# Performance work log

Hardware: AMD Instinct MI355X
Metric: run time of the kernel (lower is better)

## Reference

```python
import jax, jax.numpy as jnp
import numpy as np

N = 20000
E = 320000
IN_FEATS = 512
H = 4
D_HID = 256
D_OUT = 256
NEG_SLOPE = 0.2


def _gat_layer(h, src, dst, Wsrc, Wdst, al, ar, b, apply_act):
    # h: [N, Fin]; Wsrc/Wdst: [Fin, H*D]; al/ar: [H, D]; b: [H*D]
    Hh, Dd = al.shape
    fs = (h @ Wsrc).reshape(-1, Hh, Dd)  # [N, H, D] src projection
    fd = (h @ Wdst).reshape(-1, Hh, Dd)  # [N, H, D] dst projection
    el = (fs * al).sum(-1)               # [N, H]
    er = (fd * ar).sum(-1)               # [N, H]
    e = jax.nn.leaky_relu(el[src] + er[dst], NEG_SLOPE)  # [E, H]
    m = jax.lax.stop_gradient(jax.ops.segment_max(e, dst, num_segments=N))
    m = jnp.where(jnp.isfinite(m), m, 0.0)
    ex = jnp.exp(e - m[dst])
    den = jax.ops.segment_sum(ex, dst, num_segments=N)  # [N, H]
    alpha = ex / den[dst]                               # edge softmax per dst node
    msg = fs[src] * alpha[:, :, None]                   # [E, H, D]
    out = jax.ops.segment_sum(msg, dst, num_segments=N) + b.reshape(Hh, Dd)
    if apply_act:
        out = jax.nn.relu(out)
    return out  # [N, H, D]


def setup_inputs() -> dict:
    key = jax.random.key(0)
    ks = jax.random.split(key, 20)
    x = jax.random.normal(ks[0], (N, IN_FEATS), dtype=jnp.float32)
    src = jax.random.randint(ks[1], (E,), 0, N, dtype=jnp.int32)
    dst = jax.random.randint(ks[2], (E,), 0, N, dtype=jnp.int32)
    fins = [IN_FEATS, H * D_HID, H * D_HID]
    douts = [D_HID, D_HID, D_OUT]
    inp = {"x": x, "src": src, "dst": dst}
    ki = 3
    for l in range(3):
        fin, do = fins[l], douts[l]
        s = 1.0 / np.sqrt(fin)
        inp[f"Wsrc{l}"] = jax.random.normal(ks[ki], (fin, H * do), dtype=jnp.float32) * s; ki += 1
        inp[f"Wdst{l}"] = jax.random.normal(ks[ki], (fin, H * do), dtype=jnp.float32) * s; ki += 1
        inp[f"al{l}"] = jax.random.normal(ks[ki], (H, do), dtype=jnp.float32) * 0.1; ki += 1
        inp[f"ar{l}"] = jax.random.normal(ks[ki], (H, do), dtype=jnp.float32) * 0.1; ki += 1
        inp[f"b{l}"] = jnp.zeros((H * do,), dtype=jnp.float32)
    return inp


def reference(x, src, dst,
              Wsrc0, Wdst0, al0, ar0, b0,
              Wsrc1, Wdst1, al1, ar1, b1,
              Wsrc2, Wdst2, al2, ar2, b2):
    h = _gat_layer(x, src, dst, Wsrc0, Wdst0, al0, ar0, b0, True).reshape(N, -1)
    h = _gat_layer(h, src, dst, Wsrc1, Wdst1, al1, ar1, b1, True).reshape(N, -1)
    h = _gat_layer(h, src, dst, Wsrc2, Wdst2, al2, ar2, b2, False)  # [N, H, D_OUT]
    return h.mean(axis=1)  # [N, D_OUT]
```

## Files before the change

### kernel.cpp

```cpp
#include <hip/hip_runtime.h>
#include <hip/hip_bf16.h>
#include <math.h>

#define NNODES 20000
#define NPAD   20480
#define NBM    160
#define NEDGES 320000
#define HEADS  4
#define DDIM   256
#define MCOLS  1024

typedef __attribute__((ext_vector_type(8))) short short8;
typedef __attribute__((ext_vector_type(4))) float f32x4;

__device__ __forceinline__ unsigned short f2bf(float f) {
  unsigned u = __float_as_uint(f);
  unsigned r = (u + 0x7fffu + ((u >> 16) & 1u)) >> 16;
  return (unsigned short)r;
}
__device__ __forceinline__ float bf2f(unsigned short h) {
  return __uint_as_float(((unsigned)h) << 16);
}

__device__ __forceinline__ void async_ld16(void* lds, const void* g) {
  __builtin_amdgcn_global_load_lds(
      (const __attribute__((address_space(1))) unsigned int*)g,
      (__attribute__((address_space(3))) unsigned int*)lds, 16, 0, 0);
}

__global__ void k_zero(int* deg, int n) {
  int i = blockIdx.x*blockDim.x + threadIdx.x;
  if (i < n) deg[i] = 0;
}
__global__ void k_hist(const int* __restrict__ dst, int* deg, int e) {
  int i = blockIdx.x*blockDim.x + threadIdx.x;
  if (i < e) atomicAdd(&deg[dst[i]], 1);
}
__global__ void k_scan(const int* __restrict__ deg, int* row_ptr, int* cursor) {
  __shared__ int sm[1024];
  int t = threadIdx.x;
  const int CH = 20;
  int base = t*CH;
  int s = 0;
  #pragma unroll
  for (int i = 0; i < CH; ++i) { int idx = base+i; if (idx < NNODES) s += deg[idx]; }
  int val = s;
  sm[t] = s; __syncthreads();
  for (int off = 1; off < 1024; off <<= 1) {
    int add = (t >= off) ? sm[t-off] : 0;
    __syncthreads();
    val += add; sm[t] = val;
    __syncthreads();
  }
  int run = val - s;
  for (int i = 0; i < CH; ++i) {
    int idx = base+i;
    if (idx < NNODES) { row_ptr[idx] = run; cursor[idx] = run; run += deg[idx]; }
  }
  if (t == 0) row_ptr[NNODES] = NEDGES;
}
__global__ void k_fill(const int* __restrict__ src, const int* __restrict__ dst,
                       int* cursor, int* srcs_sorted, int e) {
  int i = blockIdx.x*blockDim.x + threadIdx.x;
  if (i < e) { int pos = atomicAdd(&cursor[dst[i]], 1); srcs_sorted[pos] = src[i]; }
}

__global__ void k_fold(const float* __restrict__ W, const float* __restrict__ v,
                       float* __restrict__ F, int K) {
  int wave = threadIdx.x >> 6, lane = threadIdx.x & 63;
  int p = blockIdx.x*4 + wave;
  if (p >= K*HEADS) return;
  int k = p >> 2, h = p & 3;
  const float4 wv = *(const float4*)&W[(size_t)k*MCOLS + h*DDIM + lane*4];
  const float4 av = *(const float4*)&v[h*DDIM + lane*4];
  float s = wv.x*av.x + wv.y*av.y + wv.z*av.z + wv.w*av.w;
  for (int off = 32; off; off >>= 1) s += __shfl_xor(s, off);
  if (lane == 0) F[k*HEADS + h] = s;
}

__global__ void k_cvt_a(const float* __restrict__ x, unsigned short* __restrict__ hi,
                        unsigned short* __restrict__ lo, int total, int total_pad) {
  int i = blockIdx.x*blockDim.x + threadIdx.x;
  int idx = i*4;
  if (idx >= total_pad) return;
  float4 v = (idx < total) ? *(const float4*)&x[idx] : make_float4(0.f,0.f,0.f,0.f);
  ushort4 h, l;
  h.x = f2bf(v.x); l.x = f2bf(v.x - bf2f(h.x));
  h.y = f2bf(v.y); l.y = f2bf(v.y - bf2f(h.y));
  h.z = f2bf(v.z); l.z = f2bf(v.z - bf2f(h.z));
  h.w = f2bf(v.w); l.w = f2bf(v.w - bf2f(h.w));
  *(ushort4*)&hi[idx] = h;
  *(ushort4*)&lo[idx] = l;
}

__global__ __launch_bounds__(256) void k_cvt_w(const float* __restrict__ W,
                                               unsigned short* __restrict__ Th, int K) {
  __shared__ float sm[32][33];
  int k0 = blockIdx.y*32, n0 = blockIdx.x*32;
  int t = threadIdx.x;
  int r = t >> 3, c4 = (t & 7)*4;
  *(float4*)&sm[r][c4] = *(const float4*)&W[(size_t)(k0 + r)*MCOLS + n0 + c4];
  __syncthreads();
  ushort4 h;
  h.x = f2bf(sm[c4+0][r]);
  h.y = f2bf(sm[c4+1][r]);
  h.z = f2bf(sm[c4+2][r]);
  h.w = f2bf(sm[c4+3][r]);
  *(ushort4*)&Th[(size_t)(n0 + r)*K + k0 + c4] = h;
}

__global__ void k_eler0(const float* __restrict__ x, const float* __restrict__ Wal,
                        const float* __restrict__ Wred,
                        float* __restrict__ el, float* __restrict__ er) {
  int n = blockIdx.x;
  int h = threadIdx.x >> 6, lane = threadIdx.x & 63;
  float sl = 0.f, sr = 0.f;
  for (int k = lane; k < 512; k += 64) {
    float xv = x[(size_t)n*512 + k];
    sl = fmaf(xv, Wal[k*HEADS + h], sl);
    sr = fmaf(xv, Wred[k*HEADS + h], sr);
  }
  for (int off = 32; off; off >>= 1) { sl += __shfl_xor(sl, off); sr += __shfl_xor(sr, off); }
  if (lane == 0) { el[n*HEADS + h] = sl; er[n*HEADS + h] = sr; }
}

__global__ __launch_bounds__(256, 3) void k_gemm_mfma(
    const unsigned short* __restrict__ Ah, const unsigned short* __restrict__ Al,
    const unsigned short* __restrict__ Bh,
    unsigned short* __restrict__ Fh, int K) {
  __shared__ short sAh[128*32], sAl[128*32], sBh[128*32];
  const int t = threadIdx.x;
  const int w = t >> 6, l = t & 63;
  const int b = blockIdx.x;
  const int xcd = b & 7, kk = b >> 3;
  const int bm = xcd*20 + (kk >> 3), bn = kk & 7;
  const int m0 = (w >> 1) * 64, n0 = (w & 1) * 64;

  f32x4 acc[4][4];
  #pragma unroll
  for (int i = 0; i < 4; ++i)
    #pragma unroll
    for (int j = 0; j < 4; ++j) acc[i][j] = (f32x4){0.f, 0.f, 0.f, 0.f};

  const int srow = t >> 2, koct = (t & 3) * 8;
  const size_t r64 = (size_t)64 * K;
  const unsigned short* gAh = Ah + (size_t)(bm*128 + srow)*K + koct;
  const unsigned short* gAl = Al + (size_t)(bm*128 + srow)*K + koct;
  const unsigned short* gBh = Bh + (size_t)(bn*128 + srow)*K + koct;
  char* lAh = (char*)sAh + w*1024;
  char* lAl = (char*)sAl + w*1024;
  char* lBh = (char*)sBh + w*1024;

  const int fr = l & 15, fq = l >> 4;

  for (int k0 = 0; k0 < K; k0 += 32) {
    async_ld16(lAh,        gAh + k0);
    async_ld16(lAh + 4096, gAh + k0 + r64);
    async_ld16(lAl,        gAl + k0);
    async_ld16(lAl + 4096, gAl + k0 + r64);
    async_ld16(lBh,        gBh + k0);
    async_ld16(lBh + 4096, gBh + k0 + r64);
    __syncthreads();

    short8 bhv[4];
    #pragma unroll
    for (int nt = 0; nt < 4; ++nt)
      bhv[nt] = *(const short8*)&sBh[(n0 + nt*16 + fr)*32 + fq*8];
    #pragma unroll
    for (int mt = 0; mt < 4; ++mt) {
      int off = (m0 + mt*16 + fr)*32 + fq*8;
      short8 ah = *(const short8*)&sAh[off];
      short8 al = *(const short8*)&sAl[off];
      #pragma unroll
      for (int nt = 0; nt < 4; ++nt) {
        acc[mt][nt] = __builtin_amdgcn_mfma_f32_16x16x32_bf16(ah, bhv[nt], acc[mt][nt], 0, 0, 0);
        acc[mt][nt] = __builtin_amdgcn_mfma_f32_16x16x32_bf16(al, bhv[nt], acc[mt][nt], 0, 0, 0);
      }
    }
    __syncthreads();
  }

  #pragma unroll
  for (int mt = 0; mt < 4; ++mt)
    #pragma unroll
    for (int nt = 0; nt < 4; ++nt) {
      size_t base = (size_t)(bm*128 + m0 + mt*16 + fq*4)*MCOLS + bn*128 + n0 + nt*16 + fr;
      Fh[base          ] = f2bf(acc[mt][nt][0]);
      Fh[base + MCOLS  ] = f2bf(acc[mt][nt][1]);
      Fh[base + 2*MCOLS] = f2bf(acc[mt][nt][2]);
      Fh[base + 3*MCOLS] = f2bf(acc[mt][nt][3]);
    }
}

__global__ __launch_bounds__(256) void k_agg_f(
    const unsigned short* __restrict__ fsh, const float* __restrict__ el,
    const float* __restrict__ er, const int* __restrict__ row_ptr,
    const int* __restrict__ srcs, const float* __restrict__ bias,
    const float* __restrict__ WalN, const float* __restrict__ WredN,
    unsigned short* __restrict__ Ahi, unsigned short* __restrict__ Alo,
    float* __restrict__ el_next, float* __restrict__ er_next) {
  __shared__ float red_sm[HEADS][8];
  int n = blockIdx.x;
  int h = threadIdx.x >> 6, lane = threadIdx.x & 63;
  int k0 = h*DDIM + lane*4;
  if (n >= NNODES) {
    ushort4 z = {0,0,0,0};
    *(ushort4*)&Ahi[(size_t)n*MCOLS + k0] = z;
    *(ushort4*)&Alo[(size_t)n*MCOLS + k0] = z;
    return;
  }
  int beg = row_ptr[n], end = row_ptr[n+1];
  float er_nh = er[n*HEADS + h];
  float den = 0.f;
  float4 acc = make_float4(0.f, 0.f, 0.f, 0.f);
  const unsigned short* fbase = fsh + h*DDIM + lane*4;
  int i = beg;
  for (; i + 3 < end; i += 4) {
    int s0 = srcs[i], s1 = srcs[i+1], s2 = srcs[i+2], s3 = srcs[i+3];
    float e0 = el[s0*HEADS + h] + er_nh;
    float e1 = el[s1*HEADS + h] + er_nh;
    float e2 = el[s2*HEADS + h] + er_nh;
    float e3 = el[s3*HEADS + h] + er_nh;
    const ushort4 u0 = *(const ushort4*)&fbase[(size_t)s0*MCOLS];
    const ushort4 u1 = *(const ushort4*)&fbase[(size_t)s1*MCOLS];
    const ushort4 u2 = *(const ushort4*)&fbase[(size_t)s2*MCOLS];
    const ushort4 u3 = *(const ushort4*)&fbase[(size_t)s3*MCOLS];
    e0 = e0 >= 0.f ? e0 : 0.2f*e0;  float w0 = expf(e0);
    e1 = e1 >= 0.f ? e1 : 0.2f*e1;  float w1 = expf(e1);
    e2 = e2 >= 0.f ? e2 : 0.2f*e2;  float w2 = expf(e2);
    e3 = e3 >= 0.f ? e3 : 0.2f*e3;  float w3 = expf(e3);
    den += (w0 + w1) + (w2 + w3);
    acc.x = fmaf(w0, bf2f(u0.x), fmaf(w1, bf2f(u1.x), fmaf(w2, bf2f(u2.x), fmaf(w3, bf2f(u3.x), acc.x))));
    acc.y = fmaf(w0, bf2f(u0.y), fmaf(w1, bf2f(u1.y), fmaf(w2, bf2f(u2.y), fmaf(w3, bf2f(u3.y), acc.y))));
    acc.z = fmaf(w0, bf2f(u0.z), fmaf(w1, bf2f(u1.z), fmaf(w2, bf2f(u2.z), fmaf(w3, bf2f(u3.z), acc.z))));
    acc.w = fmaf(w0, bf2f(u0.w), fmaf(w1, bf2f(u1.w), fmaf(w2, bf2f(u2.w), fmaf(w3, bf2f(u3.w), acc.w))));
  }
  for (; i < end; ++i) {
    int s = srcs[i];
    float e = el[s*HEADS + h] + er_nh;
    e = e >= 0.f ? e : 0.2f*e;
    float wgt = expf(e);
    den += wgt;
    const ushort4 u = *(const ushort4*)&fbase[(size_t)s*MCOLS];
    acc.x = fmaf(wgt, bf2f(u.x), acc.x);
    acc.y = fmaf(wgt, bf2f(u.y), acc.y);
    acc.z = fmaf(wgt, bf2f(u.z), acc.z);
    acc.w = fmaf(wgt, bf2f(u.w), acc.w);
  }
  float inv = den > 0.f ? 1.f/den : 0.f;
  const float4 bv = *(const float4*)&bias[k0];
  float4 o;
  o.x = fmaxf(acc.x*inv + bv.x, 0.f);
  o.y = fmaxf(acc.y*inv + bv.y, 0.f);
  o.z = fmaxf(acc.z*inv + bv.z, 0.f);
  o.w = fmaxf(acc.w*inv + bv.w, 0.f);
  ushort4 hv, lv;
  hv.x = f2bf(o.x); lv.x = f2bf(o.x - bf2f(hv.x));
  hv.y = f2bf(o.y); lv.y = f2bf(o.y - bf2f(hv.y));
  hv.z = f2bf(o.z); lv.z = f2bf(o.z - bf2f(hv.z));
  hv.w = f2bf(o.w); lv.w = f2bf(o.w - bf2f(hv.w));
  *(ushort4*)&Ahi[(size_t)n*MCOLS + k0] = hv;
  *(ushort4*)&Alo[(size_t)n*MCOLS + k0] = lv;
  const float4 a0 = *(const float4*)&WalN[(k0+0)*HEADS];
  const float4 a1 = *(const float4*)&WalN[(k0+1)*HEADS];
  const float4 a2 = *(const float4*)&WalN[(k0+2)*HEADS];
  const float4 a3 = *(const float4*)&WalN[(k0+3)*HEADS];
  const float4 q0 = *(const float4*)&WredN[(k0+0)*HEADS];
  const float4 q1 = *(const float4*)&WredN[(k0+1)*HEADS];
  const float4 q2 = *(const float4*)&WredN[(k0+2)*HEADS];
  const float4 q3 = *(const float4*)&WredN[(k0+3)*HEADS];
  float p[8];
  p[0] = o.x*a0.x + o.y*a1.x + o.z*a2.x + o.w*a3.x;
  p[1] = o.x*a0.y + o.y*a1.y + o.z*a2.y + o.w*a3.y;
  p[2] = o.x*a0.z + o.y*a1.z + o.z*a2.z + o.w*a3.z;
  p[3] = o.x*a0.w + o.y*a1.w + o.z*a2.w + o.w*a3.w;
  p[4] = o.x*q0.x + o.y*q1.x + o.z*q2.x + o.w*q3.x;
  p[5] = o.x*q0.y + o.y*q1.y + o.z*q2.y + o.w*q3.y;
  p[6] = o.x*q0.z + o.y*q1.z + o.z*q2.z + o.w*q3.z;
  p[7] = o.x*q0.w + o.y*q1.w + o.z*q2.w + o.w*q3.w;
  for (int off = 32; off; off >>= 1)
    #pragma unroll
    for (int j = 0; j < 8; ++j) p[j] += __shfl_xor(p[j], off);
  if (lane == 0)
    #pragma unroll
    for (int j = 0; j < 8; ++j) red_sm[h][j] = p[j];
  __syncthreads();
  if (threadIdx.x < 8) {
    int t = threadIdx.x;
    float v = (red_sm[0][t] + red_sm[1][t]) + (red_sm[2][t] + red_sm[3][t]);
    if (t < 4) el_next[n*HEADS + t] = v;
    else       er_next[n*HEADS + (t-4)] = v;
  }
}

__global__ __launch_bounds__(256) void k_agg_out(
    const unsigned short* __restrict__ fsh, const float* __restrict__ el,
    const float* __restrict__ er, const int* __restrict__ row_ptr,
    const int* __restrict__ srcs, const float* __restrict__ bias,
    float* __restrict__ out) {
  __shared__ float sm[HEADS*DDIM];
  int n = blockIdx.x;
  int h = threadIdx.x >> 6, lane = threadIdx.x & 63;
  int beg = row_ptr[n], end = row_ptr[n+1];
  float er_nh = er[n*HEADS + h];
  float den = 0.f;
  float4 acc = make_float4(0.f, 0.f, 0.f, 0.f);
  const unsigned short* fbase = fsh + h*DDIM + lane*4;
  int i = beg;
  for (; i + 3 < end; i += 4) {
    int s0 = srcs[i], s1 = srcs[i+1], s2 = srcs[i+2], s3 = srcs[i+3];
    float e0 = el[s0*HEADS + h] + er_nh;
    float e1 = el[s1*HEADS + h] + er_nh;
    float e2 = el[s2*HEADS + h] + er_nh;
    float e3 = el[s3*HEADS + h] + er_nh;
    const ushort4 u0 = *(const ushort4*)&fbase[(size_t)s0*MCOLS];
    const ushort4 u1 = *(const ushort4*)&fbase[(size_t)s1*MCOLS];
    const ushort4 u2 = *(const ushort4*)&fbase[(size_t)s2*MCOLS];
    const ushort4 u3 = *(const ushort4*)&fbase[(size_t)s3*MCOLS];
    e0 = e0 >= 0.f ? e0 : 0.2f*e0;  float w0 = expf(e0);
    e1 = e1 >= 0.f ? e1 : 0.2f*e1;  float w1 = expf(e1);
    e2 = e2 >= 0.f ? e2 : 0.2f*e2;  float w2 = expf(e2);
    e3 = e3 >= 0.f ? e3 : 0.2f*e3;  float w3 = expf(e3);
    den += (w0 + w1) + (w2 + w3);
    acc.x = fmaf(w0, bf2f(u0.x), fmaf(w1, bf2f(u1.x), fmaf(w2, bf2f(u2.x), fmaf(w3, bf2f(u3.x), acc.x))));
    acc.y = fmaf(w0, bf2f(u0.y), fmaf(w1, bf2f(u1.y), fmaf(w2, bf2f(u2.y), fmaf(w3, bf2f(u3.y), acc.y))));
    acc.z = fmaf(w0, bf2f(u0.z), fmaf(w1, bf2f(u1.z), fmaf(w2, bf2f(u2.z), fmaf(w3, bf2f(u3.z), acc.z))));
    acc.w = fmaf(w0, bf2f(u0.w), fmaf(w1, bf2f(u1.w), fmaf(w2, bf2f(u2.w), fmaf(w3, bf2f(u3.w), acc.w))));
  }
  for (; i < end; ++i) {
    int s = srcs[i];
    float e = el[s*HEADS + h] + er_nh;
    e = e >= 0.f ? e : 0.2f*e;
    float wgt = expf(e);
    den += wgt;
    const ushort4 u = *(const ushort4*)&fbase[(size_t)s*MCOLS];
    acc.x = fmaf(wgt, bf2f(u.x), acc.x);
    acc.y = fmaf(wgt, bf2f(u.y), acc.y);
    acc.z = fmaf(wgt, bf2f(u.z), acc.z);
    acc.w = fmaf(wgt, bf2f(u.w), acc.w);
  }
  float inv = den > 0.f ? 1.f/den : 0.f;
  const float4 bv = *(const float4*)&bias[h*DDIM + lane*4];
  acc.x = acc.x*inv + bv.x;
  acc.y = acc.y*inv + bv.y;
  acc.z = acc.z*inv + bv.z;
  acc.w = acc.w*inv + bv.w;
  *(float4*)&sm[h*DDIM + lane*4] = acc;
  __syncthreads();
  int t = threadIdx.x;
  out[(size_t)n*DDIM + t] =
      0.25f*((sm[t] + sm[DDIM + t]) + (sm[2*DDIM + t] + sm[3*DDIM + t]));
}

extern "C" void kernel_launch(void* const* d_in, const int* in_sizes, int n_in,
                              void* d_out, int out_size, void* d_ws, size_t ws_size,
                              hipStream_t stream) {
  const float* x   = (const float*)d_in[0];
  const int*   src = (const int*)d_in[1];
  const int*   dst = (const int*)d_in[2];
  const float* Wsrc[3] = {(const float*)d_in[3], (const float*)d_in[8],  (const float*)d_in[13]};
  const float* Wdst[3] = {(const float*)d_in[4], (const float*)d_in[9],  (const float*)d_in[14]};
  const float* al[3]   = {(const float*)d_in[5], (const float*)d_in[10], (const float*)d_in[15]};
  const float* ar[3]   = {(const float*)d_in[6], (const float*)d_in[11], (const float*)d_in[16]};
  const float* bb[3]   = {(const float*)d_in[7], (const float*)d_in[12], (const float*)d_in[17]};

  char* ws = (char*)d_ws;
  size_t off = 0;
  auto alloc = [&](size_t bytes) { void* p = ws + off; off += (bytes + 255) & ~255ull; return p; };
  unsigned short* fshB = (unsigned short*)alloc((size_t)NPAD*MCOLS*2);
  unsigned short* Ahi = (unsigned short*)alloc((size_t)NPAD*MCOLS*2);
  unsigned short* Alo = (unsigned short*)alloc((size_t)NPAD*MCOLS*2);
  unsigned short* Wth = (unsigned short*)alloc((size_t)MCOLS*MCOLS*2);
  float* elA  = (float*)alloc((size_t)NNODES*HEADS*4);
  float* elB  = (float*)alloc((size_t)NNODES*HEADS*4);
  float* erA  = (float*)alloc((size_t)NNODES*HEADS*4);
  float* erB  = (float*)alloc((size_t)NNODES*HEADS*4);
  float* WredB[3]; float* WalB[3];
  for (int l = 0; l < 3; ++l) {
    WredB[l] = (float*)alloc(1024*HEADS*4);
    WalB[l]  = (float*)alloc(1024*HEADS*4);
  }
  int* deg     = (int*)alloc((size_t)NNODES*4);
  int* row_ptr = (int*)alloc((size_t)(NNODES+1)*4);
  int* cursor  = (int*)alloc((size_t)NNODES*4);
  int* srcs    = (int*)alloc((size_t)NEDGES*4);
  (void)ws_size; (void)in_sizes; (void)n_in; (void)out_size;

  k_zero<<<(NNODES+255)/256, 256, 0, stream>>>(deg, NNODES);
  k_hist<<<(NEDGES+255)/256, 256, 0, stream>>>(dst, deg, NEDGES);
  k_scan<<<1, 1024, 0, stream>>>(deg, row_ptr, cursor);
  k_fill<<<(NEDGES+255)/256, 256, 0, stream>>>(src, dst, cursor, srcs, NEDGES);

  const int Fin[3] = {512, 1024, 1024};
  for (int l = 0; l < 3; ++l) {
    k_fold<<<Fin[l], 256, 0, stream>>>(Wdst[l], ar[l], WredB[l], Fin[l]);
    k_fold<<<Fin[l], 256, 0, stream>>>(Wsrc[l], al[l], WalB[l], Fin[l]);
  }

  k_cvt_a<<<(NPAD*512/4 + 255)/256, 256, 0, stream>>>(x, Ahi, Alo, NNODES*512, NPAD*512);
  k_eler0<<<NNODES, 256, 0, stream>>>(x, WalB[0], WredB[0], elA, erA);

  float* el_cur = elA; float* el_nxt = elB;
  float* er_cur = erA; float* er_nxt = erB;
  for (int l = 0; l < 3; ++l) {
    int K = Fin[l];
    dim3 gw(MCOLS/32, K/32);
    k_cvt_w<<<gw, 256, 0, stream>>>(Wsrc[l], Wth, K);
    k_gemm_mfma<<<NBM*8, 256, 0, stream>>>(Ahi, Alo, Wth, fshB, K);
    if (l < 2) {
      k_agg_f<<<NPAD, 256, 0, stream>>>(fshB, el_cur, er_cur, row_ptr, srcs, bb[l],
                                        WalB[l+1], WredB[l+1], Ahi, Alo, el_nxt, er_nxt);
      float* t1 = el_cur; el_cur = el_nxt; el_nxt = t1;
      float* t2 = er_cur; er_cur = er_nxt; er_nxt = t2;
    } else {
      k_agg_out<<<NNODES, 256, 0, stream>>>(fshB, el_cur, er_cur, row_ptr, srcs, bb[l],
                                            (float*)d_out);
    }
  }
}
```

Baseline: 807.5 us.

## Precompute per-edge attention weights in a separate kernel before aggregation

Adds a k_wgt kernel that computes exp(leaky_relu(el[src]+er[dst])) once per edge and head into a buffer, using a dst array now also written by k_fill. The aggregation kernels then read these precomputed weights instead of gathering el and computing exp, and they address features through 32-bit byte offsets. The goal is to take the redundant el gathers and exp work off the latency-bound aggregation loop. The cost is an extra launch plus writing and re-reading a 5 MB weight buffer per layer, and __expf is less precise than expf.

```diff
diff --git a/kernel.cpp b/kernel.cpp
--- a/kernel.cpp
+++ b/kernel.cpp
@@ -60,9 +60,25 @@
   if (t == 0) row_ptr[NNODES] = NEDGES;
 }
 __global__ void k_fill(const int* __restrict__ src, const int* __restrict__ dst,
-                       int* cursor, int* srcs_sorted, int e) {
+                       int* cursor, int* srcs_sorted, int* dsts_sorted, int e) {
   int i = blockIdx.x*blockDim.x + threadIdx.x;
-  if (i < e) { int pos = atomicAdd(&cursor[dst[i]], 1); srcs_sorted[pos] = src[i]; }
+  if (i < e) {
+    int d = dst[i];
+    int pos = atomicAdd(&cursor[d], 1);
+    srcs_sorted[pos] = src[i];
+    dsts_sorted[pos] = d;
+  }
+}
+
+__global__ void k_wgt(const float* __restrict__ el, const float* __restrict__ er,
+                      const int* __restrict__ srcs, const int* __restrict__ dsts,
+                      float* __restrict__ w, int e4) {
+  int i = blockIdx.x*blockDim.x + threadIdx.x;
+  if (i >= e4) return;
+  int pos = i >> 2, h = i & 3;
+  float v = el[srcs[pos]*HEADS + h] + er[dsts[pos]*HEADS + h];
+  v = v >= 0.f ? v : 0.2f*v;
+  w[i] = __expf(v);
 }
 
 __global__ void k_fold(const float* __restrict__ W, const float* __restrict__ v,
@@ -193,9 +209,9 @@
 }
 
 __global__ __launch_bounds__(256) void k_agg_f(
-    const unsigned short* __restrict__ fsh, const float* __restrict__ el,
-    const float* __restrict__ er, const int* __restrict__ row_ptr,
-    const int* __restrict__ srcs, const float* __restrict__ bias,
+    const unsigned short* __restrict__ fsh, const float* __restrict__ wbuf,
+    const int* __restrict__ row_ptr, const int* __restrict__ srcs,
+    const float* __restrict__ bias,
     const float* __restrict__ WalN, const float* __restrict__ WredN,
     unsigned short* __restrict__ Ahi, unsigned short* __restrict__ Alo,
     float* __restrict__ el_next, float* __restrict__ er_next) {
@@ -210,25 +226,24 @@
     return;
   }
   int beg = row_ptr[n], end = row_ptr[n+1];
-  float er_nh = er[n*HEADS + h];
   float den = 0.f;
   float4 acc = make_float4(0.f, 0.f, 0.f, 0.f);
-  const unsigned short* fbase = fsh + h*DDIM + lane*4;
+  const char* fbyte = (const char*)fsh;
+  const unsigned tb = (unsigned)(k0*2);
   int i = beg;
   for (; i + 3 < end; i += 4) {
-    int s0 = srcs[i], s1 = srcs[i+1], s2 = srcs[i+2], s3 = srcs[i+3];
-    float e0 = el[s0*HEADS + h] + er_nh;
-    float e1 = el[s1*HEADS + h] + er_nh;
-    float e2 = el[s2*HEADS + h] + er_nh;
-    float e3 = el[s3*HEADS + h] + er_nh;
-    const ushort4 u0 = *(const ushort4*)&fbase[(size_t)s0*MCOLS];
-    const ushort4 u1 = *(const ushort4*)&fbase[(size_t)s1*MCOLS];
-    const ushort4 u2 = *(const ushort4*)&fbase[(size_t)s2*MCOLS];
-    const ushort4 u3 = *(const ushort4*)&fbase[(size_t)s3*MCOLS];
-    e0 = e0 >= 0.f ? e0 : 0.2f*e0;  float w0 = expf(e0);
-    e1 = e1 >= 0.f ? e1 : 0.2f*e1;  float w1 = expf(e1);
-    e2 = e2 >= 0.f ? e2 : 0.2f*e2;  float w2 = expf(e2);
-    e3 = e3 >= 0.f ? e3 : 0.2f*e3;  float w3 = expf(e3);
+    float w0 = wbuf[(size_t)(i  )*HEADS + h];
+    float w1 = wbuf[(size_t)(i+1)*HEADS + h];
+    float w2 = wbuf[(size_t)(i+2)*HEADS + h];
+    float w3 = wbuf[(size_t)(i+3)*HEADS + h];
+    unsigned o0 = (unsigned)srcs[i  ]*2048u + tb;
+    unsigned o1 = (unsigned)srcs[i+1]*2048u + tb;
+    unsigned o2 = (unsigned)srcs[i+2]*2048u + tb;
+    unsigned o3 = (unsigned)srcs[i+3]*2048u + tb;
+    const ushort4 u0 = *(const ushort4*)(fbyte + o0);
+    const ushort4 u1 = *(const ushort4*)(fbyte + o1);
+    const ushort4 u2 = *(const ushort4*)(fbyte + o2);
+    const ushort4 u3 = *(const ushort4*)(fbyte + o3);
     den += (w0 + w1) + (w2 + w3);
     acc.x = fmaf(w0, bf2f(u0.x), fmaf(w1, bf2f(u1.x), fmaf(w2, bf2f(u2.x), fmaf(w3, bf2f(u3.x), acc.x))));
     acc.y = fmaf(w0, bf2f(u0.y), fmaf(w1, bf2f(u1.y), fmaf(w2, bf2f(u2.y), fmaf(w3, bf2f(u3.y), acc.y))));
@@ -236,12 +251,10 @@
     acc.w = fmaf(w0, bf2f(u0.w), fmaf(w1, bf2f(u1.w), fmaf(w2, bf2f(u2.w), fmaf(w3, bf2f(u3.w), acc.w))));
   }
   for (; i < end; ++i) {
-    int s = srcs[i];
-    float e = el[s*HEADS + h] + er_nh;
-    e = e >= 0.f ? e : 0.2f*e;
-    float wgt = expf(e);
+    float wgt = wbuf[(size_t)i*HEADS + h];
+    unsigned o = (unsigned)srcs[i]*2048u + tb;
+    const ushort4 u = *(const ushort4*)(fbyte + o);
     den += wgt;
-    const ushort4 u = *(const ushort4*)&fbase[(size_t)s*MCOLS];
     acc.x = fmaf(wgt, bf2f(u.x), acc.x);
     acc.y = fmaf(wgt, bf2f(u.y), acc.y);
     acc.z = fmaf(wgt, bf2f(u.z), acc.z);
@@ -294,33 +307,31 @@
 }
 
 __global__ __launch_bounds__(256) void k_agg_out(
-    const unsigned short* __restrict__ fsh, const float* __restrict__ el,
-    const float* __restrict__ er, const int* __restrict__ row_ptr,
-    const int* __restrict__ srcs, const float* __restrict__ bias,
-    float* __restrict__ out) {
+    const unsigned short* __restrict__ fsh, const float* __restrict__ wbuf,
+    const int* __restrict__ row_ptr, const int* __restrict__ srcs,
+    const float* __restrict__ bias, float* __restrict__ out) {
   __shared__ float sm[HEADS*DDIM];
   int n = blockIdx.x;
   int h = threadIdx.x >> 6, lane = threadIdx.x & 63;
   int beg = row_ptr[n], end = row_ptr[n+1];
-  float er_nh = er[n*HEADS + h];
   float den = 0.f;
   float4 acc = make_float4(0.f, 0.f, 0.f, 0.f);
-  const unsigned short* fbase = fsh + h*DDIM + lane*4;
+  const char* fbyte = (const char*)fsh;
+  const unsigned tb = (unsigned)((h*DDIM + lane*4)*2);
   int i = beg;
   for (; i + 3 < end; i += 4) {
-    int s0 = srcs[i], s1 = srcs[i+1], s2 = srcs[i+2], s3 = srcs[i+3];
-    float e0 = el[s0*HEADS + h] + er_nh;
-    float e1 = el[s1*HEADS + h] + er_nh;
-    float e2 = el[s2*HEADS + h] + er_nh;
-    float e3 = el[s3*HEADS + h] + er_nh;
-    const ushort4 u0 = *(const ushort4*)&fbase[(size_t)s0*MCOLS];
-    const ushort4 u1 = *(const ushort4*)&fbase[(size_t)s1*MCOLS];
-    const ushort4 u2 = *(const ushort4*)&fbase[(size_t)s2*MCOLS];
-    const ushort4 u3 = *(const ushort4*)&fbase[(size_t)s3*MCOLS];
-    e0 = e0 >= 0.f ? e0 : 0.2f*e0;  float w0 = expf(e0);
-    e1 = e1 >= 0.f ? e1 : 0.2f*e1;  float w1 = expf(e1);
-    e2 = e2 >= 0.f ? e2 : 0.2f*e2;  float w2 = expf(e2);
-    e3 = e3 >= 0.f ? e3 : 0.2f*e3;  float w3 = expf(e3);
+    float w0 = wbuf[(size_t)(i  )*HEADS + h];
+    float w1 = wbuf[(size_t)(i+1)*HEADS + h];
+    float w2 = wbuf[(size_t)(i+2)*HEADS + h];
+    float w3 = wbuf[(size_t)(i+3)*HEADS + h];
+    unsigned o0 = (unsigned)srcs[i  ]*2048u + tb;
+    unsigned o1 = (unsigned)srcs[i+1]*2048u + tb;
+    unsigned o2 = (unsigned)srcs[i+2]*2048u + tb;
+    unsigned o3 = (unsigned)srcs[i+3]*2048u + tb;
+    const ushort4 u0 = *(const ushort4*)(fbyte + o0);
+    const ushort4 u1 = *(const ushort4*)(fbyte + o1);
+    const ushort4 u2 = *(const ushort4*)(fbyte + o2);
+    const ushort4 u3 = *(const ushort4*)(fbyte + o3);
     den += (w0 + w1) + (w2 + w3);
     acc.x = fmaf(w0, bf2f(u0.x), fmaf(w1, bf2f(u1.x), fmaf(w2, bf2f(u2.x), fmaf(w3, bf2f(u3.x), acc.x))));
     acc.y = fmaf(w0, bf2f(u0.y), fmaf(w1, bf2f(u1.y), fmaf(w2, bf2f(u2.y), fmaf(w3, bf2f(u3.y), acc.y))));
@@ -328,12 +339,10 @@
     acc.w = fmaf(w0, bf2f(u0.w), fmaf(w1, bf2f(u1.w), fmaf(w2, bf2f(u2.w), fmaf(w3, bf2f(u3.w), acc.w))));
   }
   for (; i < end; ++i) {
-    int s = srcs[i];
-    float e = el[s*HEADS + h] + er_nh;
-    e = e >= 0.f ? e : 0.2f*e;
-    float wgt = expf(e);
+    float wgt = wbuf[(size_t)i*HEADS + h];
+    unsigned o = (unsigned)srcs[i]*2048u + tb;
+    const ushort4 u = *(const ushort4*)(fbyte + o);
     den += wgt;
-    const ushort4 u = *(const ushort4*)&fbase[(size_t)s*MCOLS];
     acc.x = fmaf(wgt, bf2f(u.x), acc.x);
     acc.y = fmaf(wgt, bf2f(u.y), acc.y);
     acc.z = fmaf(wgt, bf2f(u.z), acc.z);
@@ -375,6 +384,7 @@
   float* elB  = (float*)alloc((size_t)NNODES*HEADS*4);
   float* erA  = (float*)alloc((size_t)NNODES*HEADS*4);
   float* erB  = (float*)alloc((size_t)NNODES*HEADS*4);
+  float* wbuf = (float*)alloc((size_t)NEDGES*HEADS*4);
   float* WredB[3]; float* WalB[3];
   for (int l = 0; l < 3; ++l) {
     WredB[l] = (float*)alloc(1024*HEADS*4);
@@ -384,12 +394,13 @@
   int* row_ptr = (int*)alloc((size_t)(NNODES+1)*4);
   int* cursor  = (int*)alloc((size_t)NNODES*4);
   int* srcs    = (int*)alloc((size_t)NEDGES*4);
+  int* dsts    = (int*)alloc((size_t)NEDGES*4);
   (void)ws_size; (void)in_sizes; (void)n_in; (void)out_size;
 
   k_zero<<<(NNODES+255)/256, 256, 0, stream>>>(deg, NNODES);
   k_hist<<<(NEDGES+255)/256, 256, 0, stream>>>(dst, deg, NEDGES);
   k_scan<<<1, 1024, 0, stream>>>(deg, row_ptr, cursor);
-  k_fill<<<(NEDGES+255)/256, 256, 0, stream>>>(src, dst, cursor, srcs, NEDGES);
+  k_fill<<<(NEDGES+255)/256, 256, 0, stream>>>(src, dst, cursor, srcs, dsts, NEDGES);
 
   const int Fin[3] = {512, 1024, 1024};
   for (int l = 0; l < 3; ++l) {
@@ -402,18 +413,20 @@
 
   float* el_cur = elA; float* el_nxt = elB;
   float* er_cur = erA; float* er_nxt = erB;
+  const int E4 = NEDGES*HEADS;
   for (int l = 0; l < 3; ++l) {
     int K = Fin[l];
     dim3 gw(MCOLS/32, K/32);
     k_cvt_w<<<gw, 256, 0, stream>>>(Wsrc[l], Wth, K);
     k_gemm_mfma<<<NBM*8, 256, 0, stream>>>(Ahi, Alo, Wth, fshB, K);
+    k_wgt<<<(E4 + 255)/256, 256, 0, stream>>>(el_cur, er_cur, srcs, dsts, wbuf, E4);
     if (l < 2) {
-      k_agg_f<<<NPAD, 256, 0, stream>>>(fshB, el_cur, er_cur, row_ptr, srcs, bb[l],
+      k_agg_f<<<NPAD, 256, 0, stream>>>(fshB, wbuf, row_ptr, srcs, bb[l],
                                         WalB[l+1], WredB[l+1], Ahi, Alo, el_nxt, er_nxt);
       float* t1 = el_cur; el_cur = el_nxt; el_nxt = t1;
       float* t2 = er_cur; er_cur = er_nxt; er_nxt = t2;
     } else {
-      k_agg_out<<<NNODES, 256, 0, stream>>>(fshB, el_cur, er_cur, row_ptr, srcs, bb[l],
+      k_agg_out<<<NNODES, 256, 0, stream>>>(fshB, wbuf, row_ptr, srcs, bb[l],
                                             (float*)d_out);
     }
   }
```

Result: no change. 812.3 us (+0.6%).
